# Optimization experiments

Hardware: AMD Instinct MI355X
Metric: run time of the kernel (lower is better)

The kernel has to match this reference:

```python
import jax, jax.numpy as jnp
import numpy as np

TEMPERATURE = 0.05   # distiller.temperature
KD_WEIGHT = 1.0      # args.kd_weight
EPS = 1e-8
B, D = 128, 768


def _huber(diff):
    a = jnp.abs(diff)
    return jnp.where(a < 1.0, 0.5 * a * a, a - 0.5)


def _pairwise_sqdist(x):
    # ||xi||^2 + ||xj||^2 - 2 xi.xj  (squared euclidean, as in source)
    n2 = (x * x).sum(axis=1, keepdims=True)
    return n2 + n2.T - 2.0 * (x @ x.T)


def _distance_loss(s, t):
    ds = _pairwise_sqdist(s)          # [N,N]
    dt = _pairwise_sqdist(t)
    n = ds.shape[0]
    mask = jnp.triu(jnp.ones((n, n), bool), k=1)
    cnt = n * (n - 1) / 2.0
    mean_sd = jax.lax.stop_gradient(jnp.where(mask, ds, 0.0).sum() / cnt) + EPS
    mean_td = jnp.where(mask, dt, 0.0).sum() / cnt + EPS  # teacher is constant anyway
    loss = _huber(ds / mean_sd - dt / mean_td)
    return jnp.where(mask, loss, 0.0).sum() / cnt


def _angle_potentials(x):
    # diffs[i,j] = x[j] - x[i]; unit vectors; cos[i,j,k] = e[i,j] . e[k,j]
    diffs = x[None, :, :] - x[:, None, :]                       # [N,N,D]
    e = diffs / (jnp.linalg.norm(diffs, axis=-1, keepdims=True) + EPS)
    return jnp.einsum('ijd,kjd->ijk', e, e)                     # [N,N,N]


def _angle_loss(s, t):
    ps = _angle_potentials(s)
    pt = _angle_potentials(t)
    n = ps.shape[0]
    i = jnp.arange(n)
    # valid iff i != j, i != k, j != k  (matches the three masked diagonals)
    m = ((i[:, None, None] != i[None, :, None]) &
         (i[:, None, None] != i[None, None, :]) &
         (i[None, :, None] != i[None, None, :]))
    cnt = n * (n - 1) * (n - 2)
    return jnp.where(m, _huber(ps - pt), 0.0).sum() / cnt


def _contrastive_loss(sq, sp):
    scores = (sq @ sp.T) / TEMPERATURE                          # [B,B]
    tgt = jnp.arange(scores.shape[0])                           # * (B//B) == arange
    logZ = jax.nn.logsumexp(scores, axis=-1)
    return (logZ - jnp.take_along_axis(scores, tgt[:, None], axis=1)[:, 0]).mean()


def setup_inputs() -> dict:
    key = jax.random.key(0)
    k1, k2, k3, k4 = jax.random.split(key, 4)
    return {
        'student_qry': jax.random.normal(k1, (B, D), jnp.float32),
        'student_pos': jax.random.normal(k2, (B, D), jnp.float32),
        'teacher_qry': jax.random.normal(k3, (B, D), jnp.float32),
        'teacher_pos': jax.random.normal(k4, (B, D), jnp.float32),
    }


def reference(student_qry, student_pos, teacher_qry, teacher_pos):
    contrastive = _contrastive_loss(student_qry, student_pos)
    s = jnp.concatenate([student_qry, student_pos], axis=0)     # [2B,D]
    t = jnp.concatenate([teacher_qry, teacher_pos], axis=0)
    t = jax.lax.stop_gradient(t)                                # teacher under no_grad
    kd = 0.5 * _distance_loss(s, t) + 0.5 * _angle_loss(s, t)
    total = contrastive + KD_WEIGHT * kd
    return total, contrastive, kd
```

## Files before the change

### kernel.cpp

```cpp
#include <hip/hip_runtime.h>
#include <math.h>

#define N2   256
#define DIM  768
#define EPSF 1e-8f

#define OFF_G     0u
#define OFF_DIAG  131072u
#define OFF_TSUM  131584u
#define OFF_SLOT  131712u
#define SL_ANG  0
#define SL_DIST 512
#define SL_CON  768

typedef __attribute__((ext_vector_type(8))) short short8;
typedef __attribute__((ext_vector_type(4))) float f32x4;

__device__ inline float wave_reduce_sum(float v) {
    #pragma unroll
    for (int o = 32; o > 0; o >>= 1) v += __shfl_down(v, o, 64);
    return v;
}
__device__ inline float wave_reduce_max(float v) {
    #pragma unroll
    for (int o = 32; o > 0; o >>= 1) v = fmaxf(v, __shfl_down(v, o, 64));
    return v;
}
__device__ inline float block_reduce_sum(float v, volatile float* red) {
    float w = wave_reduce_sum(v);
    __syncthreads();
    if ((threadIdx.x & 63) == 0) red[threadIdx.x >> 6] = w;
    __syncthreads();
    return red[0] + red[1] + red[2] + red[3];
}
__device__ inline const float* rowptr(const float* q, const float* p, int r) {
    return (r < 128) ? (r * DIM + q) : ((r - 128) * DIM + p);
}
__device__ inline unsigned f2bf(float x) {
    union { float f; unsigned u; } v; v.f = x;
    return (v.u + 0x7fffu + ((v.u >> 16) & 1u)) >> 16;
}

__global__ __launch_bounds__(256) void gemm_kernel(
        const float* __restrict__ sq, const float* __restrict__ sp,
        const float* __restrict__ tq, const float* __restrict__ tp,
        float* __restrict__ ws) {
    const int b = blockIdx.x, t = threadIdx.x;
    const int mat = b & 1, tile = b >> 1;
    const int m0 = (tile >> 3) * 32, n0 = (tile & 7) * 32;
    const float* q = mat ? tq : sq;
    const float* p = mat ? tp : sp;

    __shared__ unsigned short Asb[32][104];
    __shared__ unsigned short Bsb[32][104];
    __shared__ float redg[4];

    const int srow = t >> 3, skq = (t & 7) * 12;
    const float* arow = rowptr(q, p, m0 + srow) + skq;
    const float* brow = rowptr(q, p, n0 + srow) + skq;

    float4 pa[3], pb[3];
    #pragma unroll
    for (int m = 0; m < 3; ++m) {
        pa[m] = *(const float4*)&arow[4 * m];
        pb[m] = *(const float4*)&brow[4 * m];
    }

    const int wave = t >> 6, lane = t & 63;
    const int wm = (wave >> 1) * 16, wn = (wave & 1) * 16;
    const int fr = lane & 15;
    const int fk = (lane >> 4) * 8;
    f32x4 acc = {0.f, 0.f, 0.f, 0.f};

    for (int c = 0; c < 8; ++c) {
        #pragma unroll
        for (int m = 0; m < 3; ++m) {
            uint2 ap, bp;
            ap.x = f2bf(pa[m].x) | (f2bf(pa[m].y) << 16);
            ap.y = f2bf(pa[m].z) | (f2bf(pa[m].w) << 16);
            bp.x = f2bf(pb[m].x) | (f2bf(pb[m].y) << 16);
            bp.y = f2bf(pb[m].z) | (f2bf(pb[m].w) << 16);
            *(uint2*)&Asb[srow][skq + 4 * m] = ap;
            *(uint2*)&Bsb[srow][skq + 4 * m] = bp;
        }
        __syncthreads();
        if (c < 7) {
            const int kb = (c + 1) * 96;
            #pragma unroll
            for (int m = 0; m < 3; ++m) {
                pa[m] = *(const float4*)&arow[kb + 4 * m];
                pb[m] = *(const float4*)&brow[kb + 4 * m];
            }
        }
        #pragma unroll
        for (int kc = 0; kc < 96; kc += 32) {
            const short8 a0 = *(const short8*)&Asb[wm + fr][kc + fk];
            const short8 b0 = *(const short8*)&Bsb[wn + fr][kc + fk];
            acc = __builtin_amdgcn_mfma_f32_16x16x32_bf16(a0, b0, acc, 0, 0, 0);
        }
        __syncthreads();
    }

    float* G = ws + OFF_G + (unsigned)mat * 65536u;
    const int crow0 = (lane >> 4) * 4;
    const int ccol = lane & 15;
    float ts = 0.f;
    #pragma unroll
    for (int reg = 0; reg < 4; ++reg) {
        const int row = m0 + wm + crow0 + reg;
        const int col = n0 + wn + ccol;
        G[row * 256 + col] = acc[reg];
        ts += acc[reg];
    }
    if (m0 == n0 && wm == wn && (lane >> 4) == (ccol >> 2)) {
        ws[OFF_DIAG + (unsigned)(mat * 256 + m0 + wm + ccol)] = acc[ccol & 3];
    }
    const float tsum = block_reduce_sum(ts, redg);
    if (t == 0) ws[OFF_TSUM + (unsigned)(mat * 64 + tile)] = tsum;
}

__global__ __launch_bounds__(256) void mega_kernel(float* __restrict__ ws) {
    const float* Pg = ws + OFF_G;
    const float* Dg = ws + OFF_DIAG;
    __shared__ float sGJ[16][68], sTJ[16][68], sIJ[16][68], sITJ[16][68];
    __shared__ float sGI[32][68], sTI[32][68];
    __shared__ float dgS[256], dgT[256];
    __shared__ float red1[4], red2[4], redS[1];
    const int b = blockIdx.x, t = threadIdx.x;

    if (b < 512) {
        const int k0 = (b & 3) * 64;
        const int j0 = ((b >> 2) & 15) * 16;
        const int i0 = (b >> 6) * 32;
        const int jj = t & 15, ii = t >> 4;
        const int i1 = i0 + ii, i2 = i1 + 16, j = j0 + jj;

        dgS[t] = Dg[t];
        dgT[t] = Dg[256 + t];

        const int r = t >> 4, c4 = (t & 15) * 4;
        const unsigned baseJ = (unsigned)((j0 + r) * 256 + k0 + c4);
        const float4 gjs = *(const float4*)&Pg[baseJ];
        const float4 gjt = *(const float4*)&Pg[65536u + baseJ];

        #pragma unroll
        for (int s2 = 0; s2 < 2; ++s2) {
            const int slot = t + 256 * s2;
            const int ri = slot >> 4, ci = (slot & 15) * 4;
            const unsigned base = (unsigned)((i0 + ri) * 256 + k0 + ci);
            *(float4*)&sGI[ri][ci] = *(const float4*)&Pg[base];
            *(float4*)&sTI[ri][ci] = *(const float4*)&Pg[65536u + base];
        }
        const float g1s = Pg[(unsigned)(i1 * 256 + j)];
        const float g1t = Pg[65536u + (unsigned)(i1 * 256 + j)];
        const float g2s = Pg[(unsigned)(i2 * 256 + j)];
        const float g2t = Pg[65536u + (unsigned)(i2 * 256 + j)];
        __syncthreads();

        {
            const float djs = dgS[j0 + r], djt = dgT[j0 + r];
            float4 ivs, ivt;
            const float* dS = &dgS[k0 + c4];
            const float* dT = &dgT[k0 + c4];
            ivs.x = 1.f / (sqrtf(fmaxf(djs + dS[0] - 2.f * gjs.x, 0.f)) + EPSF);
            ivs.y = 1.f / (sqrtf(fmaxf(djs + dS[1] - 2.f * gjs.y, 0.f)) + EPSF);
            ivs.z = 1.f / (sqrtf(fmaxf(djs + dS[2] - 2.f * gjs.z, 0.f)) + EPSF);
            ivs.w = 1.f / (sqrtf(fmaxf(djs + dS[3] - 2.f * gjs.w, 0.f)) + EPSF);
            ivt.x = 1.f / (sqrtf(fmaxf(djt + dT[0] - 2.f * gjt.x, 0.f)) + EPSF);
            ivt.y = 1.f / (sqrtf(fmaxf(djt + dT[1] - 2.f * gjt.y, 0.f)) + EPSF);
            ivt.z = 1.f / (sqrtf(fmaxf(djt + dT[2] - 2.f * gjt.z, 0.f)) + EPSF);
            ivt.w = 1.f / (sqrtf(fmaxf(djt + dT[3] - 2.f * gjt.w, 0.f)) + EPSF);
            *(float4*)&sGJ[r][c4] = gjs;
            *(float4*)&sTJ[r][c4] = gjt;
            *(float4*)&sIJ[r][c4] = ivs;
            *(float4*)&sITJ[r][c4] = ivt;
        }
        const float Gjj = dgS[j], Tjj = dgT[j];
        const float wis1 = 1.f / (sqrtf(fmaxf(dgS[i1] + Gjj - 2.f * g1s, 0.f)) + EPSF);
        const float wit1 = 1.f / (sqrtf(fmaxf(dgT[i1] + Tjj - 2.f * g1t, 0.f)) + EPSF);
        const float wis2 = 1.f / (sqrtf(fmaxf(dgS[i2] + Gjj - 2.f * g2s, 0.f)) + EPSF);
        const float wit2 = 1.f / (sqrtf(fmaxf(dgT[i2] + Tjj - 2.f * g2t, 0.f)) + EPSF);
        const float as1 = (Gjj - g1s) * wis1;
        const float at1 = (Tjj - g1t) * wit1;
        const float as2 = (Gjj - g2s) * wis2;
        const float at2 = (Tjj - g2t) * wit2;
        __syncthreads();

        float sum1 = 0.f, sum2 = 0.f;
        for (int c = 0; c < 64; c += 4) {
            const float4 gJ  = *(const float4*)&sGJ[jj][c];
            const float4 iJ  = *(const float4*)&sIJ[jj][c];
            const float4 tJ  = *(const float4*)&sTJ[jj][c];
            const float4 itJ = *(const float4*)&sITJ[jj][c];
            const float4 a1 = *(const float4*)&sGI[ii][c];
            const float4 b1 = *(const float4*)&sTI[ii][c];
            const float4 a2 = *(const float4*)&sGI[ii + 16][c];
            const float4 b2 = *(const float4*)&sTI[ii + 16][c];
            const float gJr[4]  = {gJ.x, gJ.y, gJ.z, gJ.w};
            const float iJr[4]  = {iJ.x, iJ.y, iJ.z, iJ.w};
            const float tJr[4]  = {tJ.x, tJ.y, tJ.z, tJ.w};
            const float itJr[4] = {itJ.x, itJ.y, itJ.z, itJ.w};
            const float a1r[4] = {a1.x, a1.y, a1.z, a1.w};
            const float b1r[4] = {b1.x, b1.y, b1.z, b1.w};
            const float a2r[4] = {a2.x, a2.y, a2.z, a2.w};
            const float b2r[4] = {b2.x, b2.y, b2.z, b2.w};
            #pragma unroll
            for (int e = 0; e < 4; ++e) {
                const float ps1 = fmaf(wis1, a1r[e] - gJr[e], as1) * iJr[e];
                const float pt1 = fmaf(wit1, b1r[e] - tJr[e], at1) * itJr[e];
                const float d1 = ps1 - pt1;
                const float ad1 = fabsf(d1);
                const float m1 = fminf(ad1, 1.f);
                sum1 = fmaf(m1, fmaf(-0.5f, m1, ad1), sum1);

                const float ps2 = fmaf(wis2, a2r[e] - gJr[e], as2) * iJr[e];
                const float pt2 = fmaf(wit2, b2r[e] - tJr[e], at2) * itJr[e];
                const float d2 = ps2 - pt2;
                const float ad2 = fabsf(d2);
                const float m2 = fminf(ad2, 1.f);
                sum2 = fmaf(m2, fmaf(-0.5f, m2, ad2), sum2);
            }
        }
        const float v = block_reduce_sum(sum1 + sum2, red1);
        if (t == 0) ws[OFF_SLOT + SL_ANG + b] = v;
    } else if (b < 768) {
        const int i = b - 512, j = t;
        const float gs  = Pg[(unsigned)(i * 256 + j)];
        const float gt  = Pg[65536u + (unsigned)(i * 256 + j)];
        const float djs = Dg[j], djt = Dg[256 + j];
        const float dis = Dg[i], dit = Dg[256 + i];
        const float ds = fmaxf(dis + djs - 2.f * gs, 0.f);
        const float dt = fmaxf(dit + djt - 2.f * gt, 0.f);

        const float tr_s = block_reduce_sum(djs, red1);
        const float tr_t = block_reduce_sum(djt, red1);
        const float tv = (t < 128) ? ws[OFF_TSUM + t] : 0.f;
        const float sum_gs = block_reduce_sum((t < 64) ? tv : 0.f, red1);
        const float sum_gt = block_reduce_sum((t >= 64) ? tv : 0.f, red1);
        const float rs = 1.f / ((256.f * tr_s - sum_gs) / 32640.f + EPSF);
        const float rt = 1.f / ((256.f * tr_t - sum_gt) / 32640.f + EPSF);

        const float dd = ds * rs - dt * rt;
        const float a = fabsf(dd);
        const float m = fminf(a, 1.f);
        const float hv = block_reduce_sum((j > i) ? m * fmaf(-0.5f, m, a) : 0.f, red1);
        if (t == 0) ws[OFF_SLOT + SL_DIST + i] = hv;
    } else {
        const int rrow = b - 768, j = t;
        const float gs = (j >= 128) ? Pg[(unsigned)(rrow * 256 + j)] : 0.f;
        const float s = (j >= 128) ? 20.f * gs : -INFINITY;
        if (j == 128 + rrow) redS[0] = s;
        float mx0 = wave_reduce_max(s);
        __syncthreads();
        if ((t & 63) == 0) red2[t >> 6] = mx0;
        __syncthreads();
        const float mx = fmaxf(fmaxf(red2[0], red2[1]), fmaxf(red2[2], red2[3]));
        const float e = block_reduce_sum((j >= 128) ? expf(s - mx) : 0.f, red1);
        if (t == 0) ws[OFF_SLOT + SL_CON + rrow] = mx + logf(e) - redS[0];
    }
}

__global__ __launch_bounds__(256) void finalize_kernel(const float* __restrict__ ws,
                                                       float* __restrict__ out) {
    __shared__ float red1[4];
    const int t = threadIdx.x;
    const float* S = ws + OFF_SLOT;
    const float a_ = block_reduce_sum(S[SL_ANG + t] + S[SL_ANG + 256 + t], red1);
    const float d_ = block_reduce_sum(S[SL_DIST + t], red1);
    const float c_ = block_reduce_sum((t < 128) ? S[SL_CON + t] : 0.f, red1);
    if (t == 0) {
        const float contrastive = c_ / 128.f;
        const float dist = d_ / 32640.f;
        const float ang = a_ / 16581120.f;
        const float kd = 0.5f * (dist + ang);
        out[0] = contrastive + kd;
        out[1] = contrastive;
        out[2] = kd;
    }
}

extern "C" void kernel_launch(void* const* d_in, const int* in_sizes, int n_in,
                              void* d_out, int out_size, void* d_ws, size_t ws_size,
                              hipStream_t stream) {
    (void)in_sizes; (void)n_in; (void)out_size; (void)ws_size;
    const float* sq = (const float*)d_in[0];
    const float* sp = (const float*)d_in[1];
    const float* tq = (const float*)d_in[2];
    const float* tp = (const float*)d_in[3];
    float* ws  = (float*)d_ws;
    float* out = (float*)d_out;

    gemm_kernel<<<128, 256, 0, stream>>>(sq, sp, tq, tp, ws);
    mega_kernel<<<896, 256, 0, stream>>>(ws);
    finalize_kernel<<<1, 256, 0, stream>>>(ws, out);
}
```

Baseline: 77.70 us.

## Fuse gemm, loss and finalize kernels into one cooperative launch with grid syncs

Merges the three separate kernel launches into a single cooperative kernel of 896 blocks that uses grid.sync() between the Gram-matrix GEMM phase, the loss phase and the final reduction. Shared memory for the two phases is overlaid with a union, and launch bounds request 4 blocks per CU so the whole grid can be resident. The aim is to remove launch gaps and inter-kernel boundaries. In exchange it adds the cost of two grid-wide barriers, and the cooperative launch needs all 896 blocks co-resident, which may fail or limit occupancy.

After: 275.3 us. 3.54x slower.

```diff
diff --git a/kernel.cpp b/kernel.cpp
--- a/kernel.cpp
+++ b/kernel.cpp
@@ -1,5 +1,8 @@
 #include <hip/hip_runtime.h>
+#include <hip/hip_cooperative_groups.h>
 #include <math.h>
+
+namespace cg = cooperative_groups;
 
 #define N2   256
 #define DIM  768
@@ -41,92 +44,94 @@
     return (v.u + 0x7fffu + ((v.u >> 16) & 1u)) >> 16;
 }
 
-__global__ __launch_bounds__(256) void gemm_kernel(
+__global__ __launch_bounds__(256, 4) void fused_kernel(
         const float* __restrict__ sq, const float* __restrict__ sp,
         const float* __restrict__ tq, const float* __restrict__ tp,
-        float* __restrict__ ws) {
+        float* __restrict__ ws, float* __restrict__ out) {
+    __shared__ union {
+        struct { unsigned short A[32][104]; unsigned short B[32][104]; } g;
+        struct { float GJ[16][68], TJ[16][68], IJ[16][68], ITJ[16][68];
+                 float GI[32][68], TI[32][68];
+                 float dgS[256], dgT[256]; } a;
+    } sm;
+    __shared__ float red1[4], red2[4], redS[1];
     const int b = blockIdx.x, t = threadIdx.x;
-    const int mat = b & 1, tile = b >> 1;
-    const int m0 = (tile >> 3) * 32, n0 = (tile & 7) * 32;
-    const float* q = mat ? tq : sq;
-    const float* p = mat ? tp : sp;
-
-    __shared__ unsigned short Asb[32][104];
-    __shared__ unsigned short Bsb[32][104];
-    __shared__ float redg[4];
-
-    const int srow = t >> 3, skq = (t & 7) * 12;
-    const float* arow = rowptr(q, p, m0 + srow) + skq;
-    const float* brow = rowptr(q, p, n0 + srow) + skq;
-
-    float4 pa[3], pb[3];
-    #pragma unroll
-    for (int m = 0; m < 3; ++m) {
-        pa[m] = *(const float4*)&arow[4 * m];
-        pb[m] = *(const float4*)&brow[4 * m];
-    }
-
-    const int wave = t >> 6, lane = t & 63;
-    const int wm = (wave >> 1) * 16, wn = (wave & 1) * 16;
-    const int fr = lane & 15;
-    const int fk = (lane >> 4) * 8;
-    f32x4 acc = {0.f, 0.f, 0.f, 0.f};
-
-    for (int c = 0; c < 8; ++c) {
+    cg::grid_group grid = cg::this_grid();
+
+    if (b < 128) {
+        const int mat = b & 1, tile = b >> 1;
+        const int m0 = (tile >> 3) * 32, n0 = (tile & 7) * 32;
+        const float* q = mat ? tq : sq;
+        const float* p = mat ? tp : sp;
+
+        const int srow = t >> 3, skq = (t & 7) * 12;
+        const float* arow = rowptr(q, p, m0 + srow) + skq;
+        const float* brow = rowptr(q, p, n0 + srow) + skq;
+
+        float4 pa[3], pb[3];
         #pragma unroll
         for (int m = 0; m < 3; ++m) {
-            uint2 ap, bp;
-            ap.x = f2bf(pa[m].x) | (f2bf(pa[m].y) << 16);
-            ap.y = f2bf(pa[m].z) | (f2bf(pa[m].w) << 16);
-            bp.x = f2bf(pb[m].x) | (f2bf(pb[m].y) << 16);
-            bp.y = f2bf(pb[m].z) | (f2bf(pb[m].w) << 16);
-            *(uint2*)&Asb[srow][skq + 4 * m] = ap;
-            *(uint2*)&Bsb[srow][skq + 4 * m] = bp;
-        }
-        __syncthreads();
-        if (c < 7) {
-            const int kb = (c + 1) * 96;
+            pa[m] = *(const float4*)&arow[4 * m];
+            pb[m] = *(const float4*)&brow[4 * m];
+        }
+
+        const int wave = t >> 6, lane = t & 63;
+        const int wm = (wave >> 1) * 16, wn = (wave & 1) * 16;
+        const int fr = lane & 15;
+        const int fk = (lane >> 4) * 8;
+        f32x4 acc = {0.f, 0.f, 0.f, 0.f};
+
+        for (int c = 0; c < 8; ++c) {
             #pragma unroll
             for (int m = 0; m < 3; ++m) {
-                pa[m] = *(const float4*)&arow[kb + 4 * m];
-                pb[m] = *(const float4*)&brow[kb + 4 * m];
+                uint2 ap, bp;
+                ap.x = f2bf(pa[m].x) | (f2bf(pa[m].y) << 16);
+                ap.y = f2bf(pa[m].z) | (f2bf(pa[m].w) << 16);
+                bp.x = f2bf(pb[m].x) | (f2bf(pb[m].y) << 16);
+                bp.y = f2bf(pb[m].z) | (f2bf(pb[m].w) << 16);
+                *(uint2*)&sm.g.A[srow][skq + 4 * m] = ap;
+                *(uint2*)&sm.g.B[srow][skq + 4 * m] = bp;
             }
-        }
+            __syncthreads();
+            if (c < 7) {
+                const int kb = (c + 1) * 96;
+                #pragma unroll
+                for (int m = 0; m < 3; ++m) {
+                    pa[m] = *(const float4*)&arow[kb + 4 * m];
+                    pb[m] = *(const float4*)&brow[kb + 4 * m];
+                }
+            }
+            #pragma unroll
+            for (int kc = 0; kc < 96; kc += 32) {
+                const short8 a0 = *(const short8*)&sm.g.A[wm + fr][kc + fk];
+                const short8 b0 = *(const short8*)&sm.g.B[wn + fr][kc + fk];
+                acc = __builtin_amdgcn_mfma_f32_16x16x32_bf16(a0, b0, acc, 0, 0, 0);
+            }
+            __syncthreads();
+        }
+
+        float* G = ws + OFF_G + (unsigned)mat * 65536u;
+        const int crow0 = (lane >> 4) * 4;
+        const int ccol = lane & 15;
+        float ts = 0.f;
         #pragma unroll
-        for (int kc = 0; kc < 96; kc += 32) {
-            const short8 a0 = *(const short8*)&Asb[wm + fr][kc + fk];
-            const short8 b0 = *(const short8*)&Bsb[wn + fr][kc + fk];
-            acc = __builtin_amdgcn_mfma_f32_16x16x32_bf16(a0, b0, acc, 0, 0, 0);
-        }
-        __syncthreads();
+        for (int reg = 0; reg < 4; ++reg) {
+            const int row = m0 + wm + crow0 + reg;
+            const int col = n0 + wn + ccol;
+            G[row * 256 + col] = acc[reg];
+            ts += acc[reg];
+        }
+        if (m0 == n0 && wm == wn && (lane >> 4) == (ccol >> 2)) {
+            ws[OFF_DIAG + (unsigned)(mat * 256 + m0 + wm + ccol)] = acc[ccol & 3];
+        }
+        const float tsum = block_reduce_sum(ts, red1);
+        if (t == 0) ws[OFF_TSUM + (unsigned)(mat * 64 + tile)] = tsum;
     }
 
-    float* G = ws + OFF_G + (unsigned)mat * 65536u;
-    const int crow0 = (lane >> 4) * 4;
-    const int ccol = lane & 15;
-    float ts = 0.f;
-    #pragma unroll
-    for (int reg = 0; reg < 4; ++reg) {
-        const int row = m0 + wm + crow0 + reg;
-        const int col = n0 + wn + ccol;
-        G[row * 256 + col] = acc[reg];
-        ts += acc[reg];
-    }
-    if (m0 == n0 && wm == wn && (lane >> 4) == (ccol >> 2)) {
-        ws[OFF_DIAG + (unsigned)(mat * 256 + m0 + wm + ccol)] = acc[ccol & 3];
-    }
-    const float tsum = block_reduce_sum(ts, redg);
-    if (t == 0) ws[OFF_TSUM + (unsigned)(mat * 64 + tile)] = tsum;
-}
-
-__global__ __launch_bounds__(256) void mega_kernel(float* __restrict__ ws) {
+    grid.sync();
+
     const float* Pg = ws + OFF_G;
     const float* Dg = ws + OFF_DIAG;
-    __shared__ float sGJ[16][68], sTJ[16][68], sIJ[16][68], sITJ[16][68];
-    __shared__ float sGI[32][68], sTI[32][68];
-    __shared__ float dgS[256], dgT[256];
-    __shared__ float red1[4], red2[4], redS[1];
-    const int b = blockIdx.x, t = threadIdx.x;
 
     if (b < 512) {
         const int k0 = (b & 3) * 64;
@@ -135,8 +140,10 @@
         const int jj = t & 15, ii = t >> 4;
         const int i1 = i0 + ii, i2 = i1 + 16, j = j0 + jj;
 
-        dgS[t] = Dg[t];
-        dgT[t] = Dg[256 + t];
+        __syncthreads();
+
+        sm.a.dgS[t] = Dg[t];
+        sm.a.dgT[t] = Dg[256 + t];
 
         const int r = t >> 4, c4 = (t & 15) * 4;
         const unsigned baseJ = (unsigned)((j0 + r) * 256 + k0 + c4);
@@ -148,8 +155,8 @@
             const int slot = t + 256 * s2;
             const int ri = slot >> 4, ci = (slot & 15) * 4;
             const unsigned base = (unsigned)((i0 + ri) * 256 + k0 + ci);
-            *(float4*)&sGI[ri][ci] = *(const float4*)&Pg[base];
-            *(float4*)&sTI[ri][ci] = *(const float4*)&Pg[65536u + base];
+            *(float4*)&sm.a.GI[ri][ci] = *(const float4*)&Pg[base];
+            *(float4*)&sm.a.TI[ri][ci] = *(const float4*)&Pg[65536u + base];
         }
         const float g1s = Pg[(unsigned)(i1 * 256 + j)];
         const float g1t = Pg[65536u + (unsigned)(i1 * 256 + j)];
@@ -158,10 +165,10 @@
         __syncthreads();
 
         {
-            const float djs = dgS[j0 + r], djt = dgT[j0 + r];
+            const float djs = sm.a.dgS[j0 + r], djt = sm.a.dgT[j0 + r];
             float4 ivs, ivt;
-            const float* dS = &dgS[k0 + c4];
-            const float* dT = &dgT[k0 + c4];
+            const float* dS = &sm.a.dgS[k0 + c4];
+            const float* dT = &sm.a.dgT[k0 + c4];
             ivs.x = 1.f / (sqrtf(fmaxf(djs + dS[0] - 2.f * gjs.x, 0.f)) + EPSF);
             ivs.y = 1.f / (sqrtf(fmaxf(djs + dS[1] - 2.f * gjs.y, 0.f)) + EPSF);
             ivs.z = 1.f / (sqrtf(fmaxf(djs + dS[2] - 2.f * gjs.z, 0.f)) + EPSF);
@@ -170,16 +177,16 @@
             ivt.y = 1.f / (sqrtf(fmaxf(djt + dT[1] - 2.f * gjt.y, 0.f)) + EPSF);
             ivt.z = 1.f / (sqrtf(fmaxf(djt + dT[2] - 2.f * gjt.z, 0.f)) + EPSF);
             ivt.w = 1.f / (sqrtf(fmaxf(djt + dT[3] - 2.f * gjt.w, 0.f)) + EPSF);
-            *(float4*)&sGJ[r][c4] = gjs;
-            *(float4*)&sTJ[r][c4] = gjt;
-            *(float4*)&sIJ[r][c4] = ivs;
-            *(float4*)&sITJ[r][c4] = ivt;
-        }
-        const float Gjj = dgS[j], Tjj = dgT[j];
-        const float wis1 = 1.f / (sqrtf(fmaxf(dgS[i1] + Gjj - 2.f * g1s, 0.f)) + EPSF);
-        const float wit1 = 1.f / (sqrtf(fmaxf(dgT[i1] + Tjj - 2.f * g1t, 0.f)) + EPSF);
-        const float wis2 = 1.f / (sqrtf(fmaxf(dgS[i2] + Gjj - 2.f * g2s, 0.f)) + EPSF);
-        const float wit2 = 1.f / (sqrtf(fmaxf(dgT[i2] + Tjj - 2.f * g2t, 0.f)) + EPSF);
+            *(float4*)&sm.a.GJ[r][c4] = gjs;
+            *(float4*)&sm.a.TJ[r][c4] = gjt;
+            *(float4*)&sm.a.IJ[r][c4] = ivs;
+            *(float4*)&sm.a.ITJ[r][c4] = ivt;
+        }
+        const float Gjj = sm.a.dgS[j], Tjj = sm.a.dgT[j];
+        const float wis1 = 1.f / (sqrtf(fmaxf(sm.a.dgS[i1] + Gjj - 2.f * g1s, 0.f)) + EPSF);
+        const float wit1 = 1.f / (sqrtf(fmaxf(sm.a.dgT[i1] + Tjj - 2.f * g1t, 0.f)) + EPSF);
+        const float wis2 = 1.f / (sqrtf(fmaxf(sm.a.dgS[i2] + Gjj - 2.f * g2s, 0.f)) + EPSF);
+        const float wit2 = 1.f / (sqrtf(fmaxf(sm.a.dgT[i2] + Tjj - 2.f * g2t, 0.f)) + EPSF);
         const float as1 = (Gjj - g1s) * wis1;
         const float at1 = (Tjj - g1t) * wit1;
         const float as2 = (Gjj - g2s) * wis2;
@@ -188,14 +195,14 @@
 
         float sum1 = 0.f, sum2 = 0.f;
         for (int c = 0; c < 64; c += 4) {
-            const float4 gJ  = *(const float4*)&sGJ[jj][c];
-            const float4 iJ  = *(const float4*)&sIJ[jj][c];
-            const float4 tJ  = *(const float4*)&sTJ[jj][c];
-            const float4 itJ = *(const float4*)&sITJ[jj][c];
-            const float4 a1 = *(const float4*)&sGI[ii][c];
-            const float4 b1 = *(const float4*)&sTI[ii][c];
-            const float4 a2 = *(const float4*)&sGI[ii + 16][c];
-            const float4 b2 = *(const float4*)&sTI[ii + 16][c];
+            const float4 gJ  = *(const float4*)&sm.a.GJ[jj][c];
+            const float4 iJ  = *(const float4*)&sm.a.IJ[jj][c];
+            const float4 tJ  = *(const float4*)&sm.a.TJ[jj][c];
+            const float4 itJ = *(const float4*)&sm.a.ITJ[jj][c];
+            const float4 a1 = *(const float4*)&sm.a.GI[ii][c];
+            const float4 b1 = *(const float4*)&sm.a.TI[ii][c];
+            const float4 a2 = *(const float4*)&sm.a.GI[ii + 16][c];
+            const float4 b2 = *(const float4*)&sm.a.TI[ii + 16][c];
             const float gJr[4]  = {gJ.x, gJ.y, gJ.z, gJ.w};
             const float iJr[4]  = {iJ.x, iJ.y, iJ.z, iJ.w};
             const float tJr[4]  = {tJ.x, tJ.y, tJ.z, tJ.w};
@@ -258,24 +265,23 @@
         const float e = block_reduce_sum((j >= 128) ? expf(s - mx) : 0.f, red1);
         if (t == 0) ws[OFF_SLOT + SL_CON + rrow] = mx + logf(e) - redS[0];
     }
-}
-
-__global__ __launch_bounds__(256) void finalize_kernel(const float* __restrict__ ws,
-                                                       float* __restrict__ out) {
-    __shared__ float red1[4];
-    const int t = threadIdx.x;
-    const float* S = ws + OFF_SLOT;
-    const float a_ = block_reduce_sum(S[SL_ANG + t] + S[SL_ANG + 256 + t], red1);
-    const float d_ = block_reduce_sum(S[SL_DIST + t], red1);
-    const float c_ = block_reduce_sum((t < 128) ? S[SL_CON + t] : 0.f, red1);
-    if (t == 0) {
-        const float contrastive = c_ / 128.f;
-        const float dist = d_ / 32640.f;
-        const float ang = a_ / 16581120.f;
-        const float kd = 0.5f * (dist + ang);
-        out[0] = contrastive + kd;
-        out[1] = contrastive;
-        out[2] = kd;
+
+    grid.sync();
+
+    if (b == 0) {
+        const float* S = ws + OFF_SLOT;
+        const float a_ = block_reduce_sum(S[SL_ANG + t] + S[SL_ANG + 256 + t], red1);
+        const float d_ = block_reduce_sum(S[SL_DIST + t], red1);
+        const float c_ = block_reduce_sum((t < 128) ? S[SL_CON + t] : 0.f, red1);
+        if (t == 0) {
+            const float contrastive = c_ / 128.f;
+            const float dist = d_ / 32640.f;
+            const float ang = a_ / 16581120.f;
+            const float kd = 0.5f * (dist + ang);
+            out[0] = contrastive + kd;
+            out[1] = contrastive;
+            out[2] = kd;
+        }
     }
 }
 
@@ -290,7 +296,8 @@
     float* ws  = (float*)d_ws;
     float* out = (float*)d_out;
 
-    gemm_kernel<<<128, 256, 0, stream>>>(sq, sp, tq, tp, ws);
-    mega_kernel<<<896, 256, 0, stream>>>(ws);
-    finalize_kernel<<<1, 256, 0, stream>>>(ws, out);
-}
+    void* args[] = { (void*)&sq, (void*)&sp, (void*)&tq, (void*)&tp,
+                     (void*)&ws, (void*)&out };
+    hipLaunchCooperativeKernel(fused_kernel, dim3(896), dim3(256),
+                               args, 0u, stream);
+}
```
